# Kernel tuning notes

Hardware: AMD Instinct MI355X
Metric: run time of the kernel (lower is better)

## Reference

```python
import jax, jax.numpy as jnp
import numpy as np

# Rs_hidden = [(16,0),(16,1)] -> 16 scalar irreps (dim 1) then 16 vector irreps (dim 3)
B, N, M = 4, 80, 16
CH = M + 3 * M  # 64 channels
RADII = jnp.linspace(0.0, 1.0, 3)
GAMMA = 1.0 / (0.5 ** 2)  # gaussian rbf width = radii spacing
EPS = 1e-6

_lc = np.zeros((3, 3, 3), np.float32)
for i, j, k in [(0, 1, 2), (1, 2, 0), (2, 0, 1)]:
    _lc[i, j, k] = 1.0
    _lc[i, k, j] = -1.0
LC = jnp.asarray(_lc)  # Levi-Civita


def _si(t, w0, w1):
    """SelfInteraction: per-l mixing of multiplicities. t: [B, mi0 + 3*mi1, ...]."""
    mi0, mi1 = w0.shape[1], w1.shape[1]
    s = t[:, :mi0]
    v = t[:, mi0:].reshape(t.shape[0], mi1, 3, *t.shape[2:])
    os = jnp.einsum('om,nm...->no...', w0, s)
    ov = jnp.einsum('om,nmi...->noi...', w1, v)
    ov = ov.reshape(ov.shape[0], ov.shape[1] * 3, *ov.shape[3:])
    return jnp.concatenate([os, ov], axis=1)


def _norm_act(t, act):
    """NormActivation: scalar irreps -> act(x); vector irreps -> x * act(||x||)/||x||. Channel axis 1."""
    s = act(t[:, :M])
    v = t[:, M:].reshape(t.shape[0], M, 3, *t.shape[2:])
    n = jnp.sqrt(jnp.sum(v * v, axis=2, keepdims=True) + EPS)
    v = (v * act(n) / n).reshape(t.shape[0], 3 * M, *t.shape[2:])
    return jnp.concatenate([s, v], axis=1)


def _gate_mul(gate, target):
    """gate_normwise_multiply: multiply each irrep block of target by the L2 norm of the
    corresponding gate block (norm over the irrep components, channel axis 1)."""
    gs = jnp.abs(gate[:, :M])
    gv = gate[:, M:].reshape(gate.shape[0], M, 3, *gate.shape[2:])
    gn = jnp.sqrt(jnp.sum(gv * gv, axis=2) + EPS)
    factor = jnp.concatenate([gs, jnp.repeat(gn, 3, axis=1)], axis=1)
    return factor * target


def _interleave(a_t, b_t):
    """Interleave per-(m,l) blocks: [a_l0, b_l0, a_l1, b_l1] -> Rs_hidden_double layout."""
    return jnp.concatenate([a_t[:, :M], b_t[:, :M], a_t[:, M:], b_t[:, M:]], axis=1)


def _kernel(h_nei_diff, w_k00, w_k10, w_k01, w_k11):
    """SE3 point kernel for l in {0,1}, J<=2. Returns K[n,b,a,d,c] with d,c in irrep layout."""
    rad = jnp.sqrt(jnp.sum(h_nei_diff ** 2, axis=-1) + EPS)      # [B,N,N]
    nh = h_nei_diff / rad[..., None]                              # unit vectors
    rbf = jnp.exp(-GAMMA * (rad[..., None] - RADII) ** 2)        # [B,N,N,3]
    K00 = jnp.einsum('uvk,...k->...uv', w_k00, rbf)              # [B,N,N,M,M]
    K10 = jnp.einsum('uvk,...k,...i->...uiv', w_k10, rbf, nh).reshape(B, N, N, 3 * M, M)
    K01 = jnp.einsum('uvk,...k,...j->...uvj', w_k01, rbf, nh).reshape(B, N, N, M, 3 * M)
    RJ = jnp.einsum('juvk,...k->j...uv', w_k11, rbf)             # [3,B,N,N,M,M]
    eye = jnp.eye(3, dtype=rbf.dtype)
    cross = jnp.einsum('ijk,...k->...ij', LC, nh)                # J=1 basis
    outer = nh[..., :, None] * nh[..., None, :] - eye / 3.0      # J=2 basis
    base = (RJ[0][..., None, None] * eye
            + RJ[1][..., None, None] * cross[..., None, None, :, :]
            + RJ[2][..., None, None] * outer[..., None, None, :, :])  # [B,N,N,u,v,i,j]
    K11 = jnp.transpose(base, (0, 1, 2, 3, 5, 4, 6)).reshape(B, N, N, 3 * M, 3 * M)
    top = jnp.concatenate([K00, K01], axis=-1)
    bot = jnp.concatenate([K10, K11], axis=-1)
    return jnp.concatenate([top, bot], axis=-2)                  # [B,N,N,CH,CH]


def setup_inputs() -> dict:
    key = jax.random.key(0)
    ks = jax.random.split(key, 16)
    sc = 0.1
    d = {
        'x': jax.random.normal(ks[0], (B, CH, N), jnp.float32),
        'h_nei': jax.random.normal(ks[1], (B, CH, N), jnp.float32),
        'h_nei_diff': jax.random.normal(ks[2], (B, N, N, 3), jnp.float32),
        'mask': jax.random.uniform(ks[3], (B, N, N), jnp.float32),
        'w_k00': jax.random.normal(ks[4], (M, M, 3), jnp.float32) * sc,
        'w_k10': jax.random.normal(ks[5], (M, M, 3), jnp.float32) * sc,
        'w_k01': jax.random.normal(ks[6], (M, M, 3), jnp.float32) * sc,
        'w_k11': jax.random.normal(ks[7], (3, M, M, 3), jnp.float32) * sc,
        'si_z_w0': jax.random.normal(ks[8], (M, 2 * M), jnp.float32) * sc,
        'si_z_w1': jax.random.normal(ks[9], (M, 2 * M), jnp.float32) * sc,
        'si_r1_w0': jax.random.normal(ks[10], (M, M), jnp.float32) * sc,
        'si_r1_w1': jax.random.normal(ks[11], (M, M), jnp.float32) * sc,
        'si_r2_w0': jax.random.normal(ks[12], (M, M), jnp.float32) * sc,
        'si_r2_w1': jax.random.normal(ks[13], (M, M), jnp.float32) * sc,
        'si_ph_w0': jax.random.normal(ks[14], (M, 2 * M), jnp.float32) * sc,
        'si_ph_w1': jax.random.normal(ks[15], (M, 2 * M), jnp.float32) * sc,
    }
    return d


def reference(x, h_nei, h_nei_diff, mask, w_k00, w_k10, w_k01, w_k11,
              si_z_w0, si_z_w1, si_r1_w0, si_r1_w1, si_r2_w0, si_r2_w1,
              si_ph_w0, si_ph_w1):
    Kmat = _kernel(h_nei_diff, w_k00, w_k10, w_k01, w_k11)
    # masked neighbor conv: h_conv[n,d,b,a] = sum_c h_nei[n,c,a] K[n,b,a,d,c] mask[n,b,a]
    h_conv = jnp.einsum('nca,nbadc,nba->ndba', h_nei, Kmat, mask)
    sum_h = h_conv.sum(axis=-1)                                   # [B,CH,N]
    z = _norm_act(_si(_interleave(x, sum_h), si_z_w0, si_z_w1), jax.nn.sigmoid)
    r1 = _si(x, si_r1_w0, si_r1_w1)                               # [B,CH,N]
    r2 = _si(h_conv.reshape(B, CH, N * N), si_r2_w0, si_r2_w1).reshape(B, CH, N, N)
    r = _norm_act(r1[:, :, None, :] + r2, jax.nn.sigmoid)         # [B,CH,N,N]
    gated = _gate_mul(r, h_conv)
    sum_g = gated.sum(axis=-1)                                    # [B,CH,N]
    pre_h = _norm_act(_si(_interleave(x, sum_g), si_ph_w0, si_ph_w1), jnp.tanh)
    new_h = sum_h + _gate_mul(z, pre_h + sum_h)
    return new_h
```

## Files before the change

### kernel.cpp

```cpp
#include <hip/hip_runtime.h>
#include <math.h>

#define Bq 4
#define Nq 80
#define CHq 64
#define GAMMAq 4.0f
#define EPSq 1e-6f
#define PCWL 100
#define NQUAD 24


__global__ __launch_bounds__(64) void se3_precomp(
    const float* __restrict__ h_nei,
    const float* __restrict__ x,
    const float* __restrict__ w00,
    const float* __restrict__ w10,
    const float* __restrict__ w01,
    const float* __restrict__ w11,
    const float* __restrict__ wr10,
    const float* __restrict__ wr11,
    const float* __restrict__ wr20,
    const float* __restrict__ wr21,
    float* __restrict__ pc)
{
    const int na = blockIdx.x;
    const int n  = na / Nq, a = na - n * Nq;
    const int t  = threadIdx.x;
    const int u  = t & 15;
    const int kk = t >> 4;

    __shared__ float hsh[64];
    __shared__ float xsh[64];
    __shared__ float pout[16][PCWL];

    hsh[t] = h_nei[(size_t)n * CHq * Nq + t * Nq + a];
    xsh[t] = x    [(size_t)n * CHq * Nq + t * Nq + a];
    __syncthreads();

    if (kk < 3) {
        const int k = kk;
        float a00 = 0.f, a10 = 0.f;
        float c[3] = {0.f,0.f,0.f}, p0[3] = {0.f,0.f,0.f};
        float p1[3] = {0.f,0.f,0.f}, p2[3] = {0.f,0.f,0.f};
#pragma unroll
        for (int v = 0; v < 16; ++v) {
            const float s = hsh[v];
            a00 += w00[(u * 16 + v) * 3 + k] * s;
            a10 += w10[(u * 16 + v) * 3 + k] * s;
            const float w01v = w01[(u * 16 + v) * 3 + k];
            const float w110 = w11[((0 * 16 + u) * 16 + v) * 3 + k];
            const float w111 = w11[((1 * 16 + u) * 16 + v) * 3 + k];
            const float w112 = w11[((2 * 16 + u) * 16 + v) * 3 + k];
#pragma unroll
            for (int j = 0; j < 3; ++j) {
                const float Vj = hsh[16 + v * 3 + j];
                c[j]  += w01v * Vj;
                p0[j] += w110 * Vj;
                p1[j] += w111 * Vj;
                p2[j] += w112 * Vj;
            }
        }
        pout[u][0 + k] = a00;
        pout[u][3 + k] = a10;
#pragma unroll
        for (int j = 0; j < 3; ++j) {
            pout[u][6  + k * 3 + j] = c[j];
            pout[u][15 + k * 3 + j] = p0[j];
            pout[u][24 + k * 3 + j] = p1[j];
            pout[u][33 + k * 3 + j] = p2[j];
        }
    } else {
        float r1s = 0.f, r1v[3] = {0.f, 0.f, 0.f};
#pragma unroll
        for (int v = 0; v < 16; ++v) {
            r1s += wr10[u * 16 + v] * xsh[v];
            const float wv = wr11[u * 16 + v];
#pragma unroll
            for (int j = 0; j < 3; ++j) r1v[j] += wv * xsh[16 + v * 3 + j];
        }
        pout[u][42] = r1s;
#pragma unroll
        for (int j = 0; j < 3; ++j) pout[u][43 + j] = r1v[j];
        pout[u][46] = 0.f; pout[u][47] = 0.f;
#pragma unroll
        for (int j = 90; j < 96; ++j) pout[u][j] = 0.f;
    }
    __syncthreads();

    for (int c = kk; c < 42; c += 4) {
        const bool scalarType = (c < 3) || (c >= 6 && c < 15);
        const float* W = scalarType ? wr20 : wr21;
        float acc = 0.f;
#pragma unroll
        for (int v = 0; v < 16; ++v) acc += W[u * 16 + v] * pout[v][c];
        pout[u][48 + c] = acc;
    }
    __syncthreads();

    {
        float4* dst = reinterpret_cast<float4*>(pc) + (size_t)na * (NQUAD * 16) + u;
#pragma unroll
        for (int i = 0; i < 6; ++i) {
            const int c4 = kk + i * 4;
            dst[c4 * 16] = make_float4(pout[u][c4 * 4 + 0], pout[u][c4 * 4 + 1],
                                       pout[u][c4 * 4 + 2], pout[u][c4 * 4 + 3]);
        }
    }
}

__global__ __launch_bounds__(256) void se3_main(
    const float* __restrict__ x,
    const float* __restrict__ hdiff,
    const float* __restrict__ mask,
    const float* __restrict__ wz0,
    const float* __restrict__ wz1,
    const float* __restrict__ wp0,
    const float* __restrict__ wp1,
    const float* __restrict__ pc,
    float* __restrict__ out)
{
    const int nb    = blockIdx.x;
    const int n     = nb / Nq;
    const int bnode = nb - n * Nq;
    const int tid   = threadIdx.x;
    const int g     = tid >> 4;
    const int u     = tid & 15;

    __shared__ float wsh[4][512];
    __shared__ float redW[4][8][16];
    __shared__ float sumHs[64], sumGs[64];

#pragma unroll
    for (int i = 0; i < 2; ++i) {
        const int idx = tid + i * 256;
        wsh[0][idx] = wz0[idx];
        wsh[1][idx] = wz1[idx];
        wsh[2][idx] = wp0[idx];
        wsh[3][idx] = wp1[idx];
    }

    float shs = 0.f, shv0 = 0.f, shv1 = 0.f, shv2 = 0.f;
    float sgs = 0.f, sgv0 = 0.f, sgv1 = 0.f, sgv2 = 0.f;

    const float* drow = hdiff + (size_t)(n * Nq + bnode) * Nq * 3;
    const float* mrow = mask  + (size_t)(n * Nq + bnode) * Nq;
    const float third = 1.0f / 3.0f;

    for (int it = 0; it < 5; ++it) {
        const int a = it * 16 + g;

        const float d0 = drow[a * 3 + 0], d1 = drow[a * 3 + 1], d2 = drow[a * 3 + 2];
        const float m  = mrow[a];

        const float rad = sqrtf(d0 * d0 + d1 * d1 + d2 * d2 + EPSq);
        const float inv = 1.0f / rad;
        const float nh0 = d0 * inv, nh1 = d1 * inv, nh2 = d2 * inv;
        float rb[3];
        rb[0] = expf(-GAMMAq * rad * rad);
        { float t1 = rad - 0.5f; rb[1] = expf(-GAMMAq * t1 * t1); }
        { float t2 = rad - 1.0f; rb[2] = expf(-GAMMAq * t2 * t2); }

        const float4* p4 = reinterpret_cast<const float4*>(pc)
                         + (size_t)(n * Nq + a) * (NQUAD * 16) + u;

        float pa[48];
#pragma unroll
        for (int i = 0; i < 12; ++i)
            *reinterpret_cast<float4*>(&pa[i * 4]) = p4[i * 16];
        float pb[44];
#pragma unroll
        for (int i = 0; i < 11; ++i)
            *reinterpret_cast<float4*>(&pb[i * 4]) = p4[(12 + i) * 16];

        float as_ = 0.f, a10 = 0.f;
        float c01[3] = {0.f,0.f,0.f}, p0[3] = {0.f,0.f,0.f};
        float p1[3] = {0.f,0.f,0.f}, p2[3] = {0.f,0.f,0.f};
        float bs_ = 0.f, b10 = 0.f;
        float bc01[3] = {0.f,0.f,0.f}, bp0[3] = {0.f,0.f,0.f};
        float bp1[3] = {0.f,0.f,0.f}, bp2[3] = {0.f,0.f,0.f};
#pragma unroll
        for (int k = 0; k < 3; ++k) {
            const float r = rb[k];
            as_ += r * pa[0 + k];
            a10 += r * pa[3 + k];
            bs_ += r * pb[0 + k];
            b10 += r * pb[3 + k];
#pragma unroll
            for (int j = 0; j < 3; ++j) {
                c01[j]  += r * pa[6  + k * 3 + j];
                p0[j]   += r * pa[15 + k * 3 + j];
                p1[j]   += r * pa[24 + k * 3 + j];
                p2[j]   += r * pa[33 + k * 3 + j];
                bc01[j] += r * pb[6  + k * 3 + j];
                bp0[j]  += r * pb[15 + k * 3 + j];
                bp1[j]  += r * pb[24 + k * 3 + j];
                bp2[j]  += r * pb[33 + k * 3 + j];
            }
        }

        const float hcs = m * (as_ + c01[0] * nh0 + c01[1] * nh1 + c01[2] * nh2);
        const float cr0 = p1[1] * nh2 - p1[2] * nh1;
        const float cr1 = p1[2] * nh0 - p1[0] * nh2;
        const float cr2 = p1[0] * nh1 - p1[1] * nh0;
        const float pd  = p2[0] * nh0 + p2[1] * nh1 + p2[2] * nh2;
        const float hv0 = m * (nh0 * a10 + p0[0] + cr0 + nh0 * pd - p2[0] * third);
        const float hv1 = m * (nh1 * a10 + p0[1] + cr1 + nh1 * pd - p2[1] * third);
        const float hv2 = m * (nh2 * a10 + p0[2] + cr2 + nh2 * pd - p2[2] * third);

        const float r2s = m * (bs_ + bc01[0] * nh0 + bc01[1] * nh1 + bc01[2] * nh2);
        const float br0 = bp1[1] * nh2 - bp1[2] * nh1;
        const float br1 = bp1[2] * nh0 - bp1[0] * nh2;
        const float br2 = bp1[0] * nh1 - bp1[1] * nh0;
        const float bpd = bp2[0] * nh0 + bp2[1] * nh1 + bp2[2] * nh2;
        const float r2v0 = m * (nh0 * b10 + bp0[0] + br0 + nh0 * bpd - bp2[0] * third);
        const float r2v1 = m * (nh1 * b10 + bp0[1] + br1 + nh1 * bpd - bp2[1] * third);
        const float r2v2 = m * (nh2 * b10 + bp0[2] + br2 + nh2 * bpd - bp2[2] * third);

        const float r1s  = pa[42];
        const float r1v0 = pa[43], r1v1 = pa[44], r1v2 = pa[45];

        const float rs  = 1.0f / (1.0f + expf(-(r1s + r2s)));
        const float wv0 = r1v0 + r2v0, wv1 = r1v1 + r2v1, wv2 = r1v2 + r2v2;
        const float nn  = sqrtf(wv0 * wv0 + wv1 * wv1 + wv2 * wv2 + EPSq);
        const float sc  = (1.0f / (1.0f + expf(-nn))) / nn;
        const float rv0 = wv0 * sc, rv1 = wv1 * sc, rv2 = wv2 * sc;
        const float fs  = fabsf(rs);
        const float fv  = sqrtf(rv0 * rv0 + rv1 * rv1 + rv2 * rv2 + EPSq);

        shs += hcs;        shv0 += hv0;      shv1 += hv1;      shv2 += hv2;
        sgs += fs * hcs;   sgv0 += fv * hv0; sgv1 += fv * hv1; sgv2 += fv * hv2;
    }

    float vals[8] = {shs, shv0, shv1, shv2, sgs, sgv0, sgv1, sgv2};
#pragma unroll
    for (int q = 0; q < 8; ++q) {
        vals[q] += __shfl_xor(vals[q], 16, 64);
        vals[q] += __shfl_xor(vals[q], 32, 64);
    }
    const int wave = tid >> 6;
    if ((tid & 63) < 16) {
#pragma unroll
        for (int q = 0; q < 8; ++q) redW[wave][q][u] = vals[q];
    }
    __syncthreads();

    if (tid < 16) {
        float tacc[8];
#pragma unroll
        for (int q = 0; q < 8; ++q)
            tacc[q] = redW[0][q][tid] + redW[1][q][tid] + redW[2][q][tid] + redW[3][q][tid];
        sumHs[tid] = tacc[0];
        sumGs[tid] = tacc[4];
#pragma unroll
        for (int j = 0; j < 3; ++j) {
            sumHs[16 + tid * 3 + j] = tacc[1 + j];
            sumGs[16 + tid * 3 + j] = tacc[5 + j];
        }
    }
    __syncthreads();

    if (tid < 16) {
        const float* xb = x + (size_t)n * CHq * Nq + bnode;

        float zs_in = 0.f, ps_in = 0.f;
        float zv[3] = {0.f, 0.f, 0.f};
        float pv[3] = {0.f, 0.f, 0.f};
#pragma unroll
        for (int mm = 0; mm < 32; ++mm) {
            float Sh, Sg;
            if (mm < 16) { const float xv = xb[mm * Nq]; Sh = xv; Sg = xv; }
            else         { Sh = sumHs[mm - 16]; Sg = sumGs[mm - 16]; }
            zs_in += wsh[0][tid * 32 + mm] * Sh;
            ps_in += wsh[2][tid * 32 + mm] * Sg;
            const float wz = wsh[1][tid * 32 + mm];
            const float wp = wsh[3][tid * 32 + mm];
#pragma unroll
            for (int j = 0; j < 3; ++j) {
                float Vh, Vg;
                if (mm < 16) { const float xv = xb[(16 + mm * 3 + j) * Nq]; Vh = xv; Vg = xv; }
                else { Vh = sumHs[16 + (mm - 16) * 3 + j]; Vg = sumGs[16 + (mm - 16) * 3 + j]; }
                zv[j] += wz * Vh;
                pv[j] += wp * Vg;
            }
        }

        const float zs  = 1.0f / (1.0f + expf(-zs_in));
        const float zn  = sqrtf(zv[0] * zv[0] + zv[1] * zv[1] + zv[2] * zv[2] + EPSq);
        const float zsc = (1.0f / (1.0f + expf(-zn))) / zn;
        const float zv0 = zv[0] * zsc, zv1 = zv[1] * zsc, zv2 = zv[2] * zsc;
        const float phs = tanhf(ps_in);
        const float pn  = sqrtf(pv[0] * pv[0] + pv[1] * pv[1] + pv[2] * pv[2] + EPSq);
        const float psc = tanhf(pn) / pn;
        const float pv0 = pv[0] * psc, pv1 = pv[1] * psc, pv2 = pv[2] * psc;
        const float gfs = fabsf(zs);
        const float gfv = sqrtf(zv0 * zv0 + zv1 * zv1 + zv2 * zv2 + EPSq);

        float* ob = out + (size_t)n * CHq * Nq + bnode;
        const float sh_s = sumHs[tid];
        ob[tid * Nq] = sh_s + gfs * (phs + sh_s);
#pragma unroll
        for (int j = 0; j < 3; ++j) {
            const float shv = sumHs[16 + tid * 3 + j];
            const float pvj = (j == 0) ? pv0 : ((j == 1) ? pv1 : pv2);
            ob[(16 + tid * 3 + j) * Nq] = shv + gfv * (pvj + shv);
        }
    }
}

extern "C" void kernel_launch(void* const* d_in, const int* in_sizes, int n_in,
                              void* d_out, int out_size, void* d_ws, size_t ws_size,
                              hipStream_t stream) {
    const float* x      = (const float*)d_in[0];
    const float* h_nei  = (const float*)d_in[1];
    const float* hdiff  = (const float*)d_in[2];
    const float* mask   = (const float*)d_in[3];
    const float* w00    = (const float*)d_in[4];
    const float* w10    = (const float*)d_in[5];
    const float* w01    = (const float*)d_in[6];
    const float* w11    = (const float*)d_in[7];
    const float* wz0    = (const float*)d_in[8];
    const float* wz1    = (const float*)d_in[9];
    const float* wr10   = (const float*)d_in[10];
    const float* wr11   = (const float*)d_in[11];
    const float* wr20   = (const float*)d_in[12];
    const float* wr21   = (const float*)d_in[13];
    const float* wp0    = (const float*)d_in[14];
    const float* wp1    = (const float*)d_in[15];
    float* out = (float*)d_out;
    float* pc  = (float*)d_ws;

    se3_precomp<<<Bq * Nq, 64, 0, stream>>>(
        h_nei, x, w00, w10, w01, w11, wr10, wr11, wr20, wr21, pc);
    se3_main<<<Bq * Nq, 256, 0, stream>>>(
        x, hdiff, mask, wz0, wz1, wp0, wp1, pc, out);
}
```

Baseline: 27.69 us.

## Reuse per-neighbor precompute across two target nodes and pack precomp blocks

The main kernel now handles two target nodes per block, loading each neighbor's precomputed coefficient vectors once and contracting them against both nodes' difference vectors. This halves the global traffic for the pc buffer and the number of blocks, at the cost of more registers and a larger reduction. The precompute kernel packs four (n,a) items per 256-thread block, and fast __expf intrinsics replace expf.

```diff
diff --git a/kernel.cpp b/kernel.cpp
--- a/kernel.cpp
+++ b/kernel.cpp
@@ -10,7 +10,7 @@
 #define NQUAD 24
 
 
-__global__ __launch_bounds__(64) void se3_precomp(
+__global__ __launch_bounds__(256) void se3_precomp(
     const float* __restrict__ h_nei,
     const float* __restrict__ x,
     const float* __restrict__ w00,
@@ -23,18 +23,19 @@
     const float* __restrict__ wr21,
     float* __restrict__ pc)
 {
-    const int na = blockIdx.x;
+    const int wv = threadIdx.x >> 6;
+    const int na = blockIdx.x * 4 + wv;
     const int n  = na / Nq, a = na - n * Nq;
-    const int t  = threadIdx.x;
-    const int u  = t & 15;
-    const int kk = t >> 4;
-
-    __shared__ float hsh[64];
-    __shared__ float xsh[64];
-    __shared__ float pout[16][PCWL];
-
-    hsh[t] = h_nei[(size_t)n * CHq * Nq + t * Nq + a];
-    xsh[t] = x    [(size_t)n * CHq * Nq + t * Nq + a];
+    const int tt = threadIdx.x & 63;
+    const int u  = tt & 15;
+    const int kk = tt >> 4;
+
+    __shared__ float hsh[4][64];
+    __shared__ float xsh[4][64];
+    __shared__ float pout[4][16][PCWL];
+
+    hsh[wv][tt] = h_nei[(size_t)n * CHq * Nq + tt * Nq + a];
+    xsh[wv][tt] = x    [(size_t)n * CHq * Nq + tt * Nq + a];
     __syncthreads();
 
     if (kk < 3) {
@@ -44,7 +45,7 @@
         float p1[3] = {0.f,0.f,0.f}, p2[3] = {0.f,0.f,0.f};
 #pragma unroll
         for (int v = 0; v < 16; ++v) {
-            const float s = hsh[v];
+            const float s = hsh[wv][v];
             a00 += w00[(u * 16 + v) * 3 + k] * s;
             a10 += w10[(u * 16 + v) * 3 + k] * s;
             const float w01v = w01[(u * 16 + v) * 3 + k];
@@ -53,37 +54,37 @@
             const float w112 = w11[((2 * 16 + u) * 16 + v) * 3 + k];
 #pragma unroll
             for (int j = 0; j < 3; ++j) {
-                const float Vj = hsh[16 + v * 3 + j];
+                const float Vj = hsh[wv][16 + v * 3 + j];
                 c[j]  += w01v * Vj;
                 p0[j] += w110 * Vj;
                 p1[j] += w111 * Vj;
                 p2[j] += w112 * Vj;
             }
         }
-        pout[u][0 + k] = a00;
-        pout[u][3 + k] = a10;
+        pout[wv][u][0 + k] = a00;
+        pout[wv][u][3 + k] = a10;
 #pragma unroll
         for (int j = 0; j < 3; ++j) {
-            pout[u][6  + k * 3 + j] = c[j];
-            pout[u][15 + k * 3 + j] = p0[j];
-            pout[u][24 + k * 3 + j] = p1[j];
-            pout[u][33 + k * 3 + j] = p2[j];
+            pout[wv][u][6  + k * 3 + j] = c[j];
+            pout[wv][u][15 + k * 3 + j] = p0[j];
+            pout[wv][u][24 + k * 3 + j] = p1[j];
+            pout[wv][u][33 + k * 3 + j] = p2[j];
         }
     } else {
         float r1s = 0.f, r1v[3] = {0.f, 0.f, 0.f};
 #pragma unroll
         for (int v = 0; v < 16; ++v) {
-            r1s += wr10[u * 16 + v] * xsh[v];
-            const float wv = wr11[u * 16 + v];
-#pragma unroll
-            for (int j = 0; j < 3; ++j) r1v[j] += wv * xsh[16 + v * 3 + j];
-        }
-        pout[u][42] = r1s;
-#pragma unroll
-        for (int j = 0; j < 3; ++j) pout[u][43 + j] = r1v[j];
-        pout[u][46] = 0.f; pout[u][47] = 0.f;
-#pragma unroll
-        for (int j = 90; j < 96; ++j) pout[u][j] = 0.f;
+            r1s += wr10[u * 16 + v] * xsh[wv][v];
+            const float wvv = wr11[u * 16 + v];
+#pragma unroll
+            for (int j = 0; j < 3; ++j) r1v[j] += wvv * xsh[wv][16 + v * 3 + j];
+        }
+        pout[wv][u][42] = r1s;
+#pragma unroll
+        for (int j = 0; j < 3; ++j) pout[wv][u][43 + j] = r1v[j];
+        pout[wv][u][46] = 0.f; pout[wv][u][47] = 0.f;
+#pragma unroll
+        for (int j = 90; j < 96; ++j) pout[wv][u][j] = 0.f;
     }
     __syncthreads();
 
@@ -92,8 +93,8 @@
         const float* W = scalarType ? wr20 : wr21;
         float acc = 0.f;
 #pragma unroll
-        for (int v = 0; v < 16; ++v) acc += W[u * 16 + v] * pout[v][c];
-        pout[u][48 + c] = acc;
+        for (int v = 0; v < 16; ++v) acc += W[u * 16 + v] * pout[wv][v][c];
+        pout[wv][u][48 + c] = acc;
     }
     __syncthreads();
 
@@ -102,10 +103,84 @@
 #pragma unroll
         for (int i = 0; i < 6; ++i) {
             const int c4 = kk + i * 4;
-            dst[c4 * 16] = make_float4(pout[u][c4 * 4 + 0], pout[u][c4 * 4 + 1],
-                                       pout[u][c4 * 4 + 2], pout[u][c4 * 4 + 3]);
-        }
-    }
+            dst[c4 * 16] = make_float4(pout[wv][u][c4 * 4 + 0], pout[wv][u][c4 * 4 + 1],
+                                       pout[wv][u][c4 * 4 + 2], pout[wv][u][c4 * 4 + 3]);
+        }
+    }
+}
+
+__device__ __forceinline__ void pair_contract(
+    const float* __restrict__ pa, const float* __restrict__ pb,
+    float d0, float d1, float d2, float m,
+    float& ohcs, float& ohv0, float& ohv1, float& ohv2,
+    float& ogcs, float& ogv0, float& ogv1, float& ogv2)
+{
+    const float rad = sqrtf(d0 * d0 + d1 * d1 + d2 * d2 + EPSq);
+    const float inv = 1.0f / rad;
+    const float nh0 = d0 * inv, nh1 = d1 * inv, nh2 = d2 * inv;
+    float rb[3];
+    rb[0] = __expf(-GAMMAq * rad * rad);
+    { float t1 = rad - 0.5f; rb[1] = __expf(-GAMMAq * t1 * t1); }
+    { float t2 = rad - 1.0f; rb[2] = __expf(-GAMMAq * t2 * t2); }
+
+    float as_ = 0.f, a10 = 0.f;
+    float c01[3] = {0.f,0.f,0.f}, p0[3] = {0.f,0.f,0.f};
+    float p1[3] = {0.f,0.f,0.f}, p2[3] = {0.f,0.f,0.f};
+    float bs_ = 0.f, b10 = 0.f;
+    float bc01[3] = {0.f,0.f,0.f}, bp0[3] = {0.f,0.f,0.f};
+    float bp1[3] = {0.f,0.f,0.f}, bp2[3] = {0.f,0.f,0.f};
+#pragma unroll
+    for (int k = 0; k < 3; ++k) {
+        const float r = rb[k];
+        as_ += r * pa[0 + k];
+        a10 += r * pa[3 + k];
+        bs_ += r * pb[0 + k];
+        b10 += r * pb[3 + k];
+#pragma unroll
+        for (int j = 0; j < 3; ++j) {
+            c01[j]  += r * pa[6  + k * 3 + j];
+            p0[j]   += r * pa[15 + k * 3 + j];
+            p1[j]   += r * pa[24 + k * 3 + j];
+            p2[j]   += r * pa[33 + k * 3 + j];
+            bc01[j] += r * pb[6  + k * 3 + j];
+            bp0[j]  += r * pb[15 + k * 3 + j];
+            bp1[j]  += r * pb[24 + k * 3 + j];
+            bp2[j]  += r * pb[33 + k * 3 + j];
+        }
+    }
+    const float third = 1.0f / 3.0f;
+
+    const float hcs = m * (as_ + c01[0] * nh0 + c01[1] * nh1 + c01[2] * nh2);
+    const float cr0 = p1[1] * nh2 - p1[2] * nh1;
+    const float cr1 = p1[2] * nh0 - p1[0] * nh2;
+    const float cr2 = p1[0] * nh1 - p1[1] * nh0;
+    const float pd  = p2[0] * nh0 + p2[1] * nh1 + p2[2] * nh2;
+    const float hv0 = m * (nh0 * a10 + p0[0] + cr0 + nh0 * pd - p2[0] * third);
+    const float hv1 = m * (nh1 * a10 + p0[1] + cr1 + nh1 * pd - p2[1] * third);
+    const float hv2 = m * (nh2 * a10 + p0[2] + cr2 + nh2 * pd - p2[2] * third);
+
+    const float r2s = m * (bs_ + bc01[0] * nh0 + bc01[1] * nh1 + bc01[2] * nh2);
+    const float br0 = bp1[1] * nh2 - bp1[2] * nh1;
+    const float br1 = bp1[2] * nh0 - bp1[0] * nh2;
+    const float br2 = bp1[0] * nh1 - bp1[1] * nh0;
+    const float bpd = bp2[0] * nh0 + bp2[1] * nh1 + bp2[2] * nh2;
+    const float r2v0 = m * (nh0 * b10 + bp0[0] + br0 + nh0 * bpd - bp2[0] * third);
+    const float r2v1 = m * (nh1 * b10 + bp0[1] + br1 + nh1 * bpd - bp2[1] * third);
+    const float r2v2 = m * (nh2 * b10 + bp0[2] + br2 + nh2 * bpd - bp2[2] * third);
+
+    const float r1s  = pa[42];
+    const float r1v0 = pa[43], r1v1 = pa[44], r1v2 = pa[45];
+
+    const float rs  = 1.0f / (1.0f + __expf(-(r1s + r2s)));
+    const float wv0 = r1v0 + r2v0, wv1 = r1v1 + r2v1, wv2 = r1v2 + r2v2;
+    const float nn  = sqrtf(wv0 * wv0 + wv1 * wv1 + wv2 * wv2 + EPSq);
+    const float sc  = (1.0f / (1.0f + __expf(-nn))) / nn;
+    const float rv0 = wv0 * sc, rv1 = wv1 * sc, rv2 = wv2 * sc;
+    const float fs  = fabsf(rs);
+    const float fv  = sqrtf(rv0 * rv0 + rv1 * rv1 + rv2 * rv2 + EPSq);
+
+    ohcs += hcs;      ohv0 += hv0;      ohv1 += hv1;      ohv2 += hv2;
+    ogcs += fs * hcs; ogv0 += fv * hv0; ogv1 += fv * hv1; ogv2 += fv * hv2;
 }
 
 __global__ __launch_bounds__(256) void se3_main(
@@ -119,16 +194,17 @@
     const float* __restrict__ pc,
     float* __restrict__ out)
 {
-    const int nb    = blockIdx.x;
-    const int n     = nb / Nq;
-    const int bnode = nb - n * Nq;
-    const int tid   = threadIdx.x;
-    const int g     = tid >> 4;
-    const int u     = tid & 15;
+    const int nb  = blockIdx.x;
+    const int n   = nb / (Nq / 2);
+    const int bp  = nb - n * (Nq / 2);
+    const int b0  = bp * 2;
+    const int tid = threadIdx.x;
+    const int g   = tid >> 4;
+    const int u   = tid & 15;
 
     __shared__ float wsh[4][512];
-    __shared__ float redW[4][8][16];
-    __shared__ float sumHs[64], sumGs[64];
+    __shared__ float redW[4][16][16];
+    __shared__ float sumHs[2][64], sumGs[2][64];
 
 #pragma unroll
     for (int i = 0; i < 2; ++i) {
@@ -139,30 +215,19 @@
         wsh[3][idx] = wp1[idx];
     }
 
-    float shs = 0.f, shv0 = 0.f, shv1 = 0.f, shv2 = 0.f;
-    float sgs = 0.f, sgv0 = 0.f, sgv1 = 0.f, sgv2 = 0.f;
-
-    const float* drow = hdiff + (size_t)(n * Nq + bnode) * Nq * 3;
-    const float* mrow = mask  + (size_t)(n * Nq + bnode) * Nq;
-    const float third = 1.0f / 3.0f;
+    float s0[8] = {0.f,0.f,0.f,0.f,0.f,0.f,0.f,0.f};
+    float s1[8] = {0.f,0.f,0.f,0.f,0.f,0.f,0.f,0.f};
+
+    const float* drow0 = hdiff + (size_t)(n * Nq + b0)     * Nq * 3;
+    const float* drow1 = hdiff + (size_t)(n * Nq + b0 + 1) * Nq * 3;
+    const float* mrow0 = mask  + (size_t)(n * Nq + b0)     * Nq;
+    const float* mrow1 = mask  + (size_t)(n * Nq + b0 + 1) * Nq;
 
     for (int it = 0; it < 5; ++it) {
         const int a = it * 16 + g;
 
-        const float d0 = drow[a * 3 + 0], d1 = drow[a * 3 + 1], d2 = drow[a * 3 + 2];
-        const float m  = mrow[a];
-
-        const float rad = sqrtf(d0 * d0 + d1 * d1 + d2 * d2 + EPSq);
-        const float inv = 1.0f / rad;
-        const float nh0 = d0 * inv, nh1 = d1 * inv, nh2 = d2 * inv;
-        float rb[3];
-        rb[0] = expf(-GAMMAq * rad * rad);
-        { float t1 = rad - 0.5f; rb[1] = expf(-GAMMAq * t1 * t1); }
-        { float t2 = rad - 1.0f; rb[2] = expf(-GAMMAq * t2 * t2); }
-
         const float4* p4 = reinterpret_cast<const float4*>(pc)
                          + (size_t)(n * Nq + a) * (NQUAD * 16) + u;
-
         float pa[48];
 #pragma unroll
         for (int i = 0; i < 12; ++i)
@@ -172,95 +237,52 @@
         for (int i = 0; i < 11; ++i)
             *reinterpret_cast<float4*>(&pb[i * 4]) = p4[(12 + i) * 16];
 
-        float as_ = 0.f, a10 = 0.f;
-        float c01[3] = {0.f,0.f,0.f}, p0[3] = {0.f,0.f,0.f};
-        float p1[3] = {0.f,0.f,0.f}, p2[3] = {0.f,0.f,0.f};
-        float bs_ = 0.f, b10 = 0.f;
-        float bc01[3] = {0.f,0.f,0.f}, bp0[3] = {0.f,0.f,0.f};
-        float bp1[3] = {0.f,0.f,0.f}, bp2[3] = {0.f,0.f,0.f};
-#pragma unroll
-        for (int k = 0; k < 3; ++k) {
-            const float r = rb[k];
-            as_ += r * pa[0 + k];
-            a10 += r * pa[3 + k];
-            bs_ += r * pb[0 + k];
-            b10 += r * pb[3 + k];
-#pragma unroll
-            for (int j = 0; j < 3; ++j) {
-                c01[j]  += r * pa[6  + k * 3 + j];
-                p0[j]   += r * pa[15 + k * 3 + j];
-                p1[j]   += r * pa[24 + k * 3 + j];
-                p2[j]   += r * pa[33 + k * 3 + j];
-                bc01[j] += r * pb[6  + k * 3 + j];
-                bp0[j]  += r * pb[15 + k * 3 + j];
-                bp1[j]  += r * pb[24 + k * 3 + j];
-                bp2[j]  += r * pb[33 + k * 3 + j];
-            }
-        }
-
-        const float hcs = m * (as_ + c01[0] * nh0 + c01[1] * nh1 + c01[2] * nh2);
-        const float cr0 = p1[1] * nh2 - p1[2] * nh1;
-        const float cr1 = p1[2] * nh0 - p1[0] * nh2;
-        const float cr2 = p1[0] * nh1 - p1[1] * nh0;
-        const float pd  = p2[0] * nh0 + p2[1] * nh1 + p2[2] * nh2;
-        const float hv0 = m * (nh0 * a10 + p0[0] + cr0 + nh0 * pd - p2[0] * third);
-        const float hv1 = m * (nh1 * a10 + p0[1] + cr1 + nh1 * pd - p2[1] * third);
-        const float hv2 = m * (nh2 * a10 + p0[2] + cr2 + nh2 * pd - p2[2] * third);
-
-        const float r2s = m * (bs_ + bc01[0] * nh0 + bc01[1] * nh1 + bc01[2] * nh2);
-        const float br0 = bp1[1] * nh2 - bp1[2] * nh1;
-        const float br1 = bp1[2] * nh0 - bp1[0] * nh2;
-        const float br2 = bp1[0] * nh1 - bp1[1] * nh0;
-        const float bpd = bp2[0] * nh0 + bp2[1] * nh1 + bp2[2] * nh2;
-        const float r2v0 = m * (nh0 * b10 + bp0[0] + br0 + nh0 * bpd - bp2[0] * third);
-        const float r2v1 = m * (nh1 * b10 + bp0[1] + br1 + nh1 * bpd - bp2[1] * third);
-        const float r2v2 = m * (nh2 * b10 + bp0[2] + br2 + nh2 * bpd - bp2[2] * third);
-
-        const float r1s  = pa[42];
-        const float r1v0 = pa[43], r1v1 = pa[44], r1v2 = pa[45];
-
-        const float rs  = 1.0f / (1.0f + expf(-(r1s + r2s)));
-        const float wv0 = r1v0 + r2v0, wv1 = r1v1 + r2v1, wv2 = r1v2 + r2v2;
-        const float nn  = sqrtf(wv0 * wv0 + wv1 * wv1 + wv2 * wv2 + EPSq);
-        const float sc  = (1.0f / (1.0f + expf(-nn))) / nn;
-        const float rv0 = wv0 * sc, rv1 = wv1 * sc, rv2 = wv2 * sc;
-        const float fs  = fabsf(rs);
-        const float fv  = sqrtf(rv0 * rv0 + rv1 * rv1 + rv2 * rv2 + EPSq);
-
-        shs += hcs;        shv0 += hv0;      shv1 += hv1;      shv2 += hv2;
-        sgs += fs * hcs;   sgv0 += fv * hv0; sgv1 += fv * hv1; sgv2 += fv * hv2;
-    }
-
-    float vals[8] = {shs, shv0, shv1, shv2, sgs, sgv0, sgv1, sgv2};
-#pragma unroll
-    for (int q = 0; q < 8; ++q) {
+        pair_contract(pa, pb, drow0[a*3+0], drow0[a*3+1], drow0[a*3+2], mrow0[a],
+                      s0[0], s0[1], s0[2], s0[3], s0[4], s0[5], s0[6], s0[7]);
+        pair_contract(pa, pb, drow1[a*3+0], drow1[a*3+1], drow1[a*3+2], mrow1[a],
+                      s1[0], s1[1], s1[2], s1[3], s1[4], s1[5], s1[6], s1[7]);
+    }
+
+    float vals[16];
+#pragma unroll
+    for (int q = 0; q < 8; ++q) { vals[q] = s0[q]; vals[8 + q] = s1[q]; }
+#pragma unroll
+    for (int q = 0; q < 16; ++q) {
         vals[q] += __shfl_xor(vals[q], 16, 64);
         vals[q] += __shfl_xor(vals[q], 32, 64);
     }
     const int wave = tid >> 6;
     if ((tid & 63) < 16) {
 #pragma unroll
-        for (int q = 0; q < 8; ++q) redW[wave][q][u] = vals[q];
+        for (int q = 0; q < 16; ++q) redW[wave][q][u] = vals[q];
     }
     __syncthreads();
 
     if (tid < 16) {
-        float tacc[8];
-#pragma unroll
-        for (int q = 0; q < 8; ++q)
+        float tacc[16];
+#pragma unroll
+        for (int q = 0; q < 16; ++q)
             tacc[q] = redW[0][q][tid] + redW[1][q][tid] + redW[2][q][tid] + redW[3][q][tid];
-        sumHs[tid] = tacc[0];
-        sumGs[tid] = tacc[4];
-#pragma unroll
-        for (int j = 0; j < 3; ++j) {
-            sumHs[16 + tid * 3 + j] = tacc[1 + j];
-            sumGs[16 + tid * 3 + j] = tacc[5 + j];
-        }
-    }
-    __syncthreads();
-
-    if (tid < 16) {
+#pragma unroll
+        for (int b = 0; b < 2; ++b) {
+            sumHs[b][tid] = tacc[b * 8 + 0];
+            sumGs[b][tid] = tacc[b * 8 + 4];
+#pragma unroll
+            for (int j = 0; j < 3; ++j) {
+                sumHs[b][16 + tid * 3 + j] = tacc[b * 8 + 1 + j];
+                sumGs[b][16 + tid * 3 + j] = tacc[b * 8 + 5 + j];
+            }
+        }
+    }
+    __syncthreads();
+
+    if (tid < 32) {
+        const int bsel  = tid >> 4;
+        const int u15   = tid & 15;
+        const int bnode = b0 + bsel;
         const float* xb = x + (size_t)n * CHq * Nq + bnode;
+        const float* SH = sumHs[bsel];
+        const float* SG = sumGs[bsel];
 
         float zs_in = 0.f, ps_in = 0.f;
         float zv[3] = {0.f, 0.f, 0.f};
@@ -269,24 +291,24 @@
         for (int mm = 0; mm < 32; ++mm) {
             float Sh, Sg;
             if (mm < 16) { const float xv = xb[mm * Nq]; Sh = xv; Sg = xv; }
-            else         { Sh = sumHs[mm - 16]; Sg = sumGs[mm - 16]; }
-            zs_in += wsh[0][tid * 32 + mm] * Sh;
-            ps_in += wsh[2][tid * 32 + mm] * Sg;
-            const float wz = wsh[1][tid * 32 + mm];
-            const float wp = wsh[3][tid * 32 + mm];
+            else         { Sh = SH[mm - 16]; Sg = SG[mm - 16]; }
+            zs_in += wsh[0][u15 * 32 + mm] * Sh;
+            ps_in += wsh[2][u15 * 32 + mm] * Sg;
+            const float wz = wsh[1][u15 * 32 + mm];
+            const float wp = wsh[3][u15 * 32 + mm];
 #pragma unroll
             for (int j = 0; j < 3; ++j) {
                 float Vh, Vg;
                 if (mm < 16) { const float xv = xb[(16 + mm * 3 + j) * Nq]; Vh = xv; Vg = xv; }
-                else { Vh = sumHs[16 + (mm - 16) * 3 + j]; Vg = sumGs[16 + (mm - 16) * 3 + j]; }
+                else { Vh = SH[16 + (mm - 16) * 3 + j]; Vg = SG[16 + (mm - 16) * 3 + j]; }
                 zv[j] += wz * Vh;
                 pv[j] += wp * Vg;
             }
         }
 
-        const float zs  = 1.0f / (1.0f + expf(-zs_in));
+        const float zs  = 1.0f / (1.0f + __expf(-zs_in));
         const float zn  = sqrtf(zv[0] * zv[0] + zv[1] * zv[1] + zv[2] * zv[2] + EPSq);
-        const float zsc = (1.0f / (1.0f + expf(-zn))) / zn;
+        const float zsc = (1.0f / (1.0f + __expf(-zn))) / zn;
         const float zv0 = zv[0] * zsc, zv1 = zv[1] * zsc, zv2 = zv[2] * zsc;
         const float phs = tanhf(ps_in);
         const float pn  = sqrtf(pv[0] * pv[0] + pv[1] * pv[1] + pv[2] * pv[2] + EPSq);
@@ -296,13 +318,13 @@
         const float gfv = sqrtf(zv0 * zv0 + zv1 * zv1 + zv2 * zv2 + EPSq);
 
         float* ob = out + (size_t)n * CHq * Nq + bnode;
-        const float sh_s = sumHs[tid];
-        ob[tid * Nq] = sh_s + gfs * (phs + sh_s);
+        const float sh_s = SH[u15];
+        ob[u15 * Nq] = sh_s + gfs * (phs + sh_s);
 #pragma unroll
         for (int j = 0; j < 3; ++j) {
-            const float shv = sumHs[16 + tid * 3 + j];
+            const float shv = SH[16 + u15 * 3 + j];
             const float pvj = (j == 0) ? pv0 : ((j == 1) ? pv1 : pv2);
-            ob[(16 + tid * 3 + j) * Nq] = shv + gfv * (pvj + shv);
+            ob[(16 + u15 * 3 + j) * Nq] = shv + gfv * (pvj + shv);
         }
     }
 }
@@ -329,8 +351,8 @@
     float* out = (float*)d_out;
     float* pc  = (float*)d_ws;
 
-    se3_precomp<<<Bq * Nq, 64, 0, stream>>>(
+    se3_precomp<<<(Bq * Nq) / 4, 256, 0, stream>>>(
         h_nei, x, w00, w10, w01, w11, wr10, wr11, wr20, wr21, pc);
-    se3_main<<<Bq * Nq, 256, 0, stream>>>(
+    se3_main<<<(Bq * Nq) / 2, 256, 0, stream>>>(
         x, hdiff, mask, wz0, wz1, wp0, wp1, pc, out);
 }
```

Result: slower. 36.31 us (+31.1%).

## Split neighbor loop across five blocks with last-block atomic reduction

Applied to the files above, without the earlier changes.

The main kernel now launches five blocks per (batch,node) instead of one, each handling 16 neighbors. Partial sums go to global slots, and an atomic counter elects the last block to do the final reduction and the self-interaction epilogue. The goal is more parallelism and latency hiding on a GPU that was underfilled with 320 blocks. In exchange it adds a memset launch, global-memory partial traffic and atomics. It also switches expf to the faster, less precise __expf.

```diff
diff --git a/kernel.cpp b/kernel.cpp
--- a/kernel.cpp
+++ b/kernel.cpp
@@ -8,6 +8,7 @@
 #define EPSq 1e-6f
 #define PCWL 100
 #define NQUAD 24
+#define NSLICE 5
 
 
 __global__ __launch_bounds__(64) void se3_precomp(
@@ -108,6 +109,80 @@
     }
 }
 
+__device__ __forceinline__ void pair_contract(
+    const float* __restrict__ pa, const float* __restrict__ pb,
+    float d0, float d1, float d2, float m,
+    float& ohcs, float& ohv0, float& ohv1, float& ohv2,
+    float& ogcs, float& ogv0, float& ogv1, float& ogv2)
+{
+    const float rad = sqrtf(d0 * d0 + d1 * d1 + d2 * d2 + EPSq);
+    const float inv = 1.0f / rad;
+    const float nh0 = d0 * inv, nh1 = d1 * inv, nh2 = d2 * inv;
+    float rb[3];
+    rb[0] = __expf(-GAMMAq * rad * rad);
+    { float t1 = rad - 0.5f; rb[1] = __expf(-GAMMAq * t1 * t1); }
+    { float t2 = rad - 1.0f; rb[2] = __expf(-GAMMAq * t2 * t2); }
+
+    float as_ = 0.f, a10 = 0.f;
+    float c01[3] = {0.f,0.f,0.f}, p0[3] = {0.f,0.f,0.f};
+    float p1[3] = {0.f,0.f,0.f}, p2[3] = {0.f,0.f,0.f};
+    float bs_ = 0.f, b10 = 0.f;
+    float bc01[3] = {0.f,0.f,0.f}, bp0[3] = {0.f,0.f,0.f};
+    float bp1[3] = {0.f,0.f,0.f}, bp2[3] = {0.f,0.f,0.f};
+#pragma unroll
+    for (int k = 0; k < 3; ++k) {
+        const float r = rb[k];
+        as_ += r * pa[0 + k];
+        a10 += r * pa[3 + k];
+        bs_ += r * pb[0 + k];
+        b10 += r * pb[3 + k];
+#pragma unroll
+        for (int j = 0; j < 3; ++j) {
+            c01[j]  += r * pa[6  + k * 3 + j];
+            p0[j]   += r * pa[15 + k * 3 + j];
+            p1[j]   += r * pa[24 + k * 3 + j];
+            p2[j]   += r * pa[33 + k * 3 + j];
+            bc01[j] += r * pb[6  + k * 3 + j];
+            bp0[j]  += r * pb[15 + k * 3 + j];
+            bp1[j]  += r * pb[24 + k * 3 + j];
+            bp2[j]  += r * pb[33 + k * 3 + j];
+        }
+    }
+    const float third = 1.0f / 3.0f;
+
+    const float hcs = m * (as_ + c01[0] * nh0 + c01[1] * nh1 + c01[2] * nh2);
+    const float cr0 = p1[1] * nh2 - p1[2] * nh1;
+    const float cr1 = p1[2] * nh0 - p1[0] * nh2;
+    const float cr2 = p1[0] * nh1 - p1[1] * nh0;
+    const float pd  = p2[0] * nh0 + p2[1] * nh1 + p2[2] * nh2;
+    const float hv0 = m * (nh0 * a10 + p0[0] + cr0 + nh0 * pd - p2[0] * third);
+    const float hv1 = m * (nh1 * a10 + p0[1] + cr1 + nh1 * pd - p2[1] * third);
+    const float hv2 = m * (nh2 * a10 + p0[2] + cr2 + nh2 * pd - p2[2] * third);
+
+    const float r2s = m * (bs_ + bc01[0] * nh0 + bc01[1] * nh1 + bc01[2] * nh2);
+    const float br0 = bp1[1] * nh2 - bp1[2] * nh1;
+    const float br1 = bp1[2] * nh0 - bp1[0] * nh2;
+    const float br2 = bp1[0] * nh1 - bp1[1] * nh0;
+    const float bpd = bp2[0] * nh0 + bp2[1] * nh1 + bp2[2] * nh2;
+    const float r2v0 = m * (nh0 * b10 + bp0[0] + br0 + nh0 * bpd - bp2[0] * third);
+    const float r2v1 = m * (nh1 * b10 + bp0[1] + br1 + nh1 * bpd - bp2[1] * third);
+    const float r2v2 = m * (nh2 * b10 + bp0[2] + br2 + nh2 * bpd - bp2[2] * third);
+
+    const float r1s  = pa[42];
+    const float r1v0 = pa[43], r1v1 = pa[44], r1v2 = pa[45];
+
+    const float rs  = 1.0f / (1.0f + __expf(-(r1s + r2s)));
+    const float wv0 = r1v0 + r2v0, wv1 = r1v1 + r2v1, wv2 = r1v2 + r2v2;
+    const float nn  = sqrtf(wv0 * wv0 + wv1 * wv1 + wv2 * wv2 + EPSq);
+    const float sc  = (1.0f / (1.0f + __expf(-nn))) / nn;
+    const float rv0 = wv0 * sc, rv1 = wv1 * sc, rv2 = wv2 * sc;
+    const float fs  = fabsf(rs);
+    const float fv  = sqrtf(rv0 * rv0 + rv1 * rv1 + rv2 * rv2 + EPSq);
+
+    ohcs += hcs;      ohv0 += hv0;      ohv1 += hv1;      ohv2 += hv2;
+    ogcs += fs * hcs; ogv0 += fv * hv0; ogv1 += fv * hv1; ogv2 += fv * hv2;
+}
+
 __global__ __launch_bounds__(256) void se3_main(
     const float* __restrict__ x,
     const float* __restrict__ hdiff,
@@ -117,18 +192,76 @@
     const float* __restrict__ wp0,
     const float* __restrict__ wp1,
     const float* __restrict__ pc,
+    float* __restrict__ slots,
+    unsigned* __restrict__ cnt,
     float* __restrict__ out)
 {
-    const int nb    = blockIdx.x;
+    const int bid   = blockIdx.x;
+    const int nb    = bid / NSLICE;
+    const int s     = bid - nb * NSLICE;
     const int n     = nb / Nq;
     const int bnode = nb - n * Nq;
     const int tid   = threadIdx.x;
     const int g     = tid >> 4;
     const int u     = tid & 15;
+    const int a     = s * 16 + g;
 
     __shared__ float wsh[4][512];
     __shared__ float redW[4][8][16];
     __shared__ float sumHs[64], sumGs[64];
+    __shared__ unsigned lastFlag;
+
+    const float* dp = hdiff + ((size_t)(n * Nq + bnode) * Nq + a) * 3;
+    const float d0 = dp[0], d1 = dp[1], d2 = dp[2];
+    const float m  = mask[(size_t)(n * Nq + bnode) * Nq + a];
+
+    const float4* p4 = reinterpret_cast<const float4*>(pc)
+                     + (size_t)(n * Nq + a) * (NQUAD * 16) + u;
+    float pa[48];
+#pragma unroll
+    for (int i = 0; i < 12; ++i)
+        *reinterpret_cast<float4*>(&pa[i * 4]) = p4[i * 16];
+    float pb[44];
+#pragma unroll
+    for (int i = 0; i < 11; ++i)
+        *reinterpret_cast<float4*>(&pb[i * 4]) = p4[(12 + i) * 16];
+
+    float vals[8] = {0.f,0.f,0.f,0.f,0.f,0.f,0.f,0.f};
+    pair_contract(pa, pb, d0, d1, d2, m,
+                  vals[0], vals[1], vals[2], vals[3],
+                  vals[4], vals[5], vals[6], vals[7]);
+
+#pragma unroll
+    for (int q = 0; q < 8; ++q) {
+        vals[q] += __shfl_xor(vals[q], 16, 64);
+        vals[q] += __shfl_xor(vals[q], 32, 64);
+    }
+    const int wave = tid >> 6;
+    if ((tid & 63) < 16) {
+#pragma unroll
+        for (int q = 0; q < 8; ++q) redW[wave][q][u] = vals[q];
+    }
+    __syncthreads();
+
+    if (tid < 16) {
+        float* slot = slots + (size_t)bid * 128;
+#pragma unroll
+        for (int q = 0; q < 8; ++q) {
+            const float t = redW[0][q][tid] + redW[1][q][tid]
+                          + redW[2][q][tid] + redW[3][q][tid];
+            __hip_atomic_store(&slot[q * 16 + tid], t,
+                               __ATOMIC_RELAXED, __HIP_MEMORY_SCOPE_AGENT);
+        }
+    }
+    __syncthreads();
+
+    if (tid == 0) {
+        const unsigned prev = __hip_atomic_fetch_add(&cnt[nb], 1u,
+                                  __ATOMIC_ACQ_REL, __HIP_MEMORY_SCOPE_AGENT);
+        lastFlag = (prev == NSLICE - 1) ? 1u : 0u;
+    }
+    __syncthreads();
+    if (!lastFlag) return;
 
 #pragma unroll
     for (int i = 0; i < 2; ++i) {
@@ -138,117 +271,16 @@
         wsh[2][idx] = wp0[idx];
         wsh[3][idx] = wp1[idx];
     }
-
-    float shs = 0.f, shv0 = 0.f, shv1 = 0.f, shv2 = 0.f;
-    float sgs = 0.f, sgv0 = 0.f, sgv1 = 0.f, sgv2 = 0.f;
-
-    const float* drow = hdiff + (size_t)(n * Nq + bnode) * Nq * 3;
-    const float* mrow = mask  + (size_t)(n * Nq + bnode) * Nq;
-    const float third = 1.0f / 3.0f;
-
-    for (int it = 0; it < 5; ++it) {
-        const int a = it * 16 + g;
-
-        const float d0 = drow[a * 3 + 0], d1 = drow[a * 3 + 1], d2 = drow[a * 3 + 2];
-        const float m  = mrow[a];
-
-        const float rad = sqrtf(d0 * d0 + d1 * d1 + d2 * d2 + EPSq);
-        const float inv = 1.0f / rad;
-        const float nh0 = d0 * inv, nh1 = d1 * inv, nh2 = d2 * inv;
-        float rb[3];
-        rb[0] = expf(-GAMMAq * rad * rad);
-        { float t1 = rad - 0.5f; rb[1] = expf(-GAMMAq * t1 * t1); }
-        { float t2 = rad - 1.0f; rb[2] = expf(-GAMMAq * t2 * t2); }
-
-        const float4* p4 = reinterpret_cast<const float4*>(pc)
-                         + (size_t)(n * Nq + a) * (NQUAD * 16) + u;
-
-        float pa[48];
-#pragma unroll
-        for (int i = 0; i < 12; ++i)
-            *reinterpret_cast<float4*>(&pa[i * 4]) = p4[i * 16];
-        float pb[44];
-#pragma unroll
-        for (int i = 0; i < 11; ++i)
-            *reinterpret_cast<float4*>(&pb[i * 4]) = p4[(12 + i) * 16];
-
-        float as_ = 0.f, a10 = 0.f;
-        float c01[3] = {0.f,0.f,0.f}, p0[3] = {0.f,0.f,0.f};
-        float p1[3] = {0.f,0.f,0.f}, p2[3] = {0.f,0.f,0.f};
-        float bs_ = 0.f, b10 = 0.f;
-        float bc01[3] = {0.f,0.f,0.f}, bp0[3] = {0.f,0.f,0.f};
-        float bp1[3] = {0.f,0.f,0.f}, bp2[3] = {0.f,0.f,0.f};
-#pragma unroll
-        for (int k = 0; k < 3; ++k) {
-            const float r = rb[k];
-            as_ += r * pa[0 + k];
-            a10 += r * pa[3 + k];
-            bs_ += r * pb[0 + k];
-            b10 += r * pb[3 + k];
-#pragma unroll
-            for (int j = 0; j < 3; ++j) {
-                c01[j]  += r * pa[6  + k * 3 + j];
-                p0[j]   += r * pa[15 + k * 3 + j];
-                p1[j]   += r * pa[24 + k * 3 + j];
-                p2[j]   += r * pa[33 + k * 3 + j];
-                bc01[j] += r * pb[6  + k * 3 + j];
-                bp0[j]  += r * pb[15 + k * 3 + j];
-                bp1[j]  += r * pb[24 + k * 3 + j];
-                bp2[j]  += r * pb[33 + k * 3 + j];
-            }
-        }
-
-        const float hcs = m * (as_ + c01[0] * nh0 + c01[1] * nh1 + c01[2] * nh2);
-        const float cr0 = p1[1] * nh2 - p1[2] * nh1;
-        const float cr1 = p1[2] * nh0 - p1[0] * nh2;
-        const float cr2 = p1[0] * nh1 - p1[1] * nh0;
-        const float pd  = p2[0] * nh0 + p2[1] * nh1 + p2[2] * nh2;
-        const float hv0 = m * (nh0 * a10 + p0[0] + cr0 + nh0 * pd - p2[0] * third);
-        const float hv1 = m * (nh1 * a10 + p0[1] + cr1 + nh1 * pd - p2[1] * third);
-        const float hv2 = m * (nh2 * a10 + p0[2] + cr2 + nh2 * pd - p2[2] * third);
-
-        const float r2s = m * (bs_ + bc01[0] * nh0 + bc01[1] * nh1 + bc01[2] * nh2);
-        const float br0 = bp1[1] * nh2 - bp1[2] * nh1;
-        const float br1 = bp1[2] * nh0 - bp1[0] * nh2;
-        const float br2 = bp1[0] * nh1 - bp1[1] * nh0;
-        const float bpd = bp2[0] * nh0 + bp2[1] * nh1 + bp2[2] * nh2;
-        const float r2v0 = m * (nh0 * b10 + bp0[0] + br0 + nh0 * bpd - bp2[0] * third);
-        const float r2v1 = m * (nh1 * b10 + bp0[1] + br1 + nh1 * bpd - bp2[1] * third);
-        const float r2v2 = m * (nh2 * b10 + bp0[2] + br2 + nh2 * bpd - bp2[2] * third);
-
-        const float r1s  = pa[42];
-        const float r1v0 = pa[43], r1v1 = pa[44], r1v2 = pa[45];
-
-        const float rs  = 1.0f / (1.0f + expf(-(r1s + r2s)));
-        const float wv0 = r1v0 + r2v0, wv1 = r1v1 + r2v1, wv2 = r1v2 + r2v2;
-        const float nn  = sqrtf(wv0 * wv0 + wv1 * wv1 + wv2 * wv2 + EPSq);
-        const float sc  = (1.0f / (1.0f + expf(-nn))) / nn;
-        const float rv0 = wv0 * sc, rv1 = wv1 * sc, rv2 = wv2 * sc;
-        const float fs  = fabsf(rs);
-        const float fv  = sqrtf(rv0 * rv0 + rv1 * rv1 + rv2 * rv2 + EPSq);
-
-        shs += hcs;        shv0 += hv0;      shv1 += hv1;      shv2 += hv2;
-        sgs += fs * hcs;   sgv0 += fv * hv0; sgv1 += fv * hv1; sgv2 += fv * hv2;
-    }
-
-    float vals[8] = {shs, shv0, shv1, shv2, sgs, sgv0, sgv1, sgv2};
-#pragma unroll
-    for (int q = 0; q < 8; ++q) {
-        vals[q] += __shfl_xor(vals[q], 16, 64);
-        vals[q] += __shfl_xor(vals[q], 32, 64);
-    }
-    const int wave = tid >> 6;
-    if ((tid & 63) < 16) {
-#pragma unroll
-        for (int q = 0; q < 8; ++q) redW[wave][q][u] = vals[q];
-    }
-    __syncthreads();
-
     if (tid < 16) {
-        float tacc[8];
-#pragma unroll
-        for (int q = 0; q < 8; ++q)
-            tacc[q] = redW[0][q][tid] + redW[1][q][tid] + redW[2][q][tid] + redW[3][q][tid];
+        float tacc[8] = {0.f,0.f,0.f,0.f,0.f,0.f,0.f,0.f};
+#pragma unroll
+        for (int ss = 0; ss < NSLICE; ++ss) {
+            const float* slot = slots + (size_t)(nb * NSLICE + ss) * 128;
+#pragma unroll
+            for (int q = 0; q < 8; ++q)
+                tacc[q] += __hip_atomic_load(&slot[q * 16 + tid],
+                               __ATOMIC_RELAXED, __HIP_MEMORY_SCOPE_AGENT);
+        }
         sumHs[tid] = tacc[0];
         sumGs[tid] = tacc[4];
 #pragma unroll
@@ -284,9 +316,9 @@
             }
         }
 
-        const float zs  = 1.0f / (1.0f + expf(-zs_in));
+        const float zs  = 1.0f / (1.0f + __expf(-zs_in));
         const float zn  = sqrtf(zv[0] * zv[0] + zv[1] * zv[1] + zv[2] * zv[2] + EPSq);
-        const float zsc = (1.0f / (1.0f + expf(-zn))) / zn;
+        const float zsc = (1.0f / (1.0f + __expf(-zn))) / zn;
         const float zv0 = zv[0] * zsc, zv1 = zv[1] * zsc, zv2 = zv[2] * zsc;
         const float phs = tanhf(ps_in);
         const float pn  = sqrtf(pv[0] * pv[0] + pv[1] * pv[1] + pv[2] * pv[2] + EPSq);
@@ -327,10 +359,15 @@
     const float* wp0    = (const float*)d_in[14];
     const float* wp1    = (const float*)d_in[15];
     float* out = (float*)d_out;
-    float* pc  = (float*)d_ws;
-
+
+    char* ws = (char*)d_ws;
+    float*    pc    = (float*)ws;
+    float*    slots = (float*)(ws + (2u << 20));
+    unsigned* cnt   = (unsigned*)(ws + (3u << 20));
+
+    hipMemsetAsync(cnt, 0, Bq * Nq * sizeof(unsigned), stream);
     se3_precomp<<<Bq * Nq, 64, 0, stream>>>(
         h_nei, x, w00, w10, w01, w11, wr10, wr11, wr20, wr21, pc);
-    se3_main<<<Bq * Nq, 256, 0, stream>>>(
-        x, hdiff, mask, wz0, wz1, wp0, wp1, pc, out);
+    se3_main<<<Bq * Nq * NSLICE, 256, 0, stream>>>(
+        x, hdiff, mask, wz0, wz1, wp0, wp1, pc, slots, cnt, out);
 }
```

After: 65.90 us. 138% more time.
